# Kernel tuning notes

Measured on AMD Instinct MI355X. Metric: run time of the kernel, lower is better.

The kernel has to match this reference:

```python
import jax, jax.numpy as jnp
import numpy as np

B, T_ENC, H, L, OUT, S_DEC = 32, 512, 512, 2, 128, 128
KV = 2 * H  # bidirectional encoder output width


def setup_inputs() -> dict:
    key = jax.random.key(0)
    ks = jax.random.split(key, 17)
    s = 0.05  # keep recurrent dynamics stable
    return {
        "encoder_output": jax.random.normal(ks[0], (B, T_ENC, KV), jnp.float32),
        "h0": jax.random.normal(ks[1], (L, B, H), jnp.float32) * s,
        "c0": jax.random.normal(ks[2], (L, B, H), jnp.float32) * s,
        "Wk": jax.random.normal(ks[3], (KV, KV), jnp.float32) * s,
        "Wq": jax.random.normal(ks[4], (KV, H), jnp.float32) * s,
        "Wv": jax.random.normal(ks[5], (KV, KV), jnp.float32) * s,
        "We": jax.random.normal(ks[6], (1, KV), jnp.float32) * s,
        "wih0": jax.random.normal(ks[7], (4 * H, OUT + KV), jnp.float32) * s,
        "whh0": jax.random.normal(ks[8], (4 * H, H), jnp.float32) * s,
        "bih0": jax.random.normal(ks[9], (4 * H,), jnp.float32) * s,
        "bhh0": jax.random.normal(ks[10], (4 * H,), jnp.float32) * s,
        "wih1": jax.random.normal(ks[11], (4 * H, H), jnp.float32) * s,
        "whh1": jax.random.normal(ks[12], (4 * H, H), jnp.float32) * s,
        "bih1": jax.random.normal(ks[13], (4 * H,), jnp.float32) * s,
        "bhh1": jax.random.normal(ks[14], (4 * H,), jnp.float32) * s,
        "fc_w": jax.random.normal(ks[15], (OUT, H), jnp.float32) * s,
        "fc_b": jax.random.normal(ks[16], (OUT,), jnp.float32) * s,
        "seq_length": S_DEC,
    }


def _lstm_cell(x, h, c, wih, whh, bih, bhh):
    # torch gate order: i, f, g, o
    g = x @ wih.T + h @ whh.T + bih + bhh
    i, f, gg, o = jnp.split(g, 4, axis=-1)
    c_new = jax.nn.sigmoid(f) * c + jax.nn.sigmoid(i) * jnp.tanh(gg)
    h_new = jax.nn.sigmoid(o) * jnp.tanh(c_new)
    return h_new, c_new


def reference(encoder_output, h0, c0, Wk, Wq, Wv, We, wih0, whh0, bih0, bhh0,
              wih1, whh1, bih1, bhh1, fc_w, fc_b, seq_length):
    # precomputed projections (key_layer / value_layer, no bias)
    key = encoder_output @ Wk.T      # [B, T_enc, KV]
    value = encoder_output @ Wv.T    # [B, T_enc, KV]

    def step(carry, _):
        h, c, y = carry  # h,c: [L,B,H]; y: [B,OUT]
        # Bahdanau attention, query = layer-0 hidden state
        q = h[0] @ Wq.T                                         # [B, KV]
        scores = jnp.einsum('btk,k->bt', jnp.tanh(q[:, None, :] + key), We[0])
        alpha = jax.nn.softmax(scores, axis=-1)                 # [B, T_enc]
        context = jnp.einsum('bt,btd->bd', alpha, value)        # [B, KV]
        x = jnp.concatenate([y, context], axis=-1)              # [B, OUT+KV]
        h0n, c0n = _lstm_cell(x, h[0], c[0], wih0, whh0, bih0, bhh0)
        h1n, c1n = _lstm_cell(h0n, h[1], c[1], wih1, whh1, bih1, bhh1)
        y_hat = jax.nn.relu(h1n @ fc_w.T + fc_b)                # [B, OUT]
        new_carry = (jnp.stack([h0n, h1n]), jnp.stack([c0n, c1n]), 1.0 + y_hat)
        return new_carry, y_hat

    y_init = jnp.zeros((h0.shape[1], fc_b.shape[0]), jnp.float32)  # SOS = 0.0
    _, ys = jax.lax.scan(step, (h0, c0, y_init), None, length=seq_length)
    return jnp.transpose(ys, (1, 0, 2))  # [B, seq_length, OUT]
```

## Files before the change

### kernel.cpp

```cpp
#include <hip/hip_runtime.h>
#include <hip/hip_bf16.h>
#include <cstdint>

#define TE    512
#define SD    128

typedef unsigned short u16;
typedef u16 u16x4 __attribute__((ext_vector_type(4)));
typedef u16 u16x8 __attribute__((ext_vector_type(8)));

#define QO    0
#define SCO   32768
#define CTXO  81920
#define YO    114688
#define H0O   118784
#define C0O   151552
#define H1O   184320
#define C1O   217088
#define ST_N  249856

__device__ __forceinline__ float b2f(u16 v) { return __uint_as_float(((unsigned)v) << 16); }
__device__ __forceinline__ u16 f2b(float f) {
  unsigned u = __float_as_uint(f);
  return (u16)((u + 0x7FFFu + ((u >> 16) & 1u)) >> 16);
}
__device__ __forceinline__ float tanh_f(float x) {
  float xc = fminf(12.f, fmaxf(-12.f, x));
  float e  = __expf(2.f * xc);
  return __fdividef(e - 1.f, e + 1.f);
}
__device__ __forceinline__ float sigm(float x) {
  float xc = fminf(30.f, fmaxf(-30.f, x));
  return __fdividef(1.f, 1.f + __expf(-xc));
}

__global__ __launch_bounds__(256)
void gemm_kv(const float* __restrict__ E, const float* __restrict__ Wk,
             const float* __restrict__ Wv, u16* __restrict__ key, u16* __restrict__ value) {
  const float* B = blockIdx.z ? Wv : Wk;
  u16* outp = blockIdx.z ? value : key;
  __shared__ float Asm[16][68], Bsm[16][68];
  const int tid = threadIdx.x;
  const int tm = blockIdx.x * 64, tn = blockIdx.y * 64;
  const int lr = tid >> 2, lc = (tid & 3) * 4;
  const int tx = tid & 15, ty = tid >> 4;
  float acc[4][4] = {};
  for (int k0 = 0; k0 < 1024; k0 += 16) {
    float4 av = *(const float4*)(&E[(long)(tm + lr) * 1024 + k0 + lc]);
    float4 bv = *(const float4*)(&B[(long)(tn + lr) * 1024 + k0 + lc]);
    Asm[lc][lr] = av.x; Asm[lc + 1][lr] = av.y; Asm[lc + 2][lr] = av.z; Asm[lc + 3][lr] = av.w;
    Bsm[lc][lr] = bv.x; Bsm[lc + 1][lr] = bv.y; Bsm[lc + 2][lr] = bv.z; Bsm[lc + 3][lr] = bv.w;
    __syncthreads();
#pragma unroll
    for (int kk = 0; kk < 16; ++kk) {
      float4 a4 = *(const float4*)(&Asm[kk][ty * 4]);
      float4 b4 = *(const float4*)(&Bsm[kk][tx * 4]);
      acc[0][0] += a4.x * b4.x; acc[0][1] += a4.x * b4.y; acc[0][2] += a4.x * b4.z; acc[0][3] += a4.x * b4.w;
      acc[1][0] += a4.y * b4.x; acc[1][1] += a4.y * b4.y; acc[1][2] += a4.y * b4.z; acc[1][3] += a4.y * b4.w;
      acc[2][0] += a4.z * b4.x; acc[2][1] += a4.z * b4.y; acc[2][2] += a4.z * b4.z; acc[2][3] += a4.z * b4.w;
      acc[3][0] += a4.w * b4.x; acc[3][1] += a4.w * b4.y; acc[3][2] += a4.w * b4.z; acc[3][3] += a4.w * b4.w;
    }
    __syncthreads();
  }
#pragma unroll
  for (int i = 0; i < 4; ++i)
#pragma unroll
    for (int j = 0; j < 4; ++j)
      outp[(long)(tm + ty * 4 + i) * 1024 + tn + tx * 4 + j] = f2b(acc[i][j]);
}

__global__ __launch_bounds__(256)
void init_state(const float* __restrict__ h0, const float* __restrict__ c0, float* __restrict__ st) {
  int i = blockIdx.x * 256 + threadIdx.x;
  st[H0O + i] = h0[i];
  st[H1O + i] = h0[16384 + i];
  st[C0O + i] = c0[i];
  st[C1O + i] = c0[16384 + i];
  if (i < 4096) st[YO + i] = 0.f;
}

__global__ __launch_bounds__(256)
void qproj(const float* __restrict__ h0, const float* __restrict__ Wq, float* __restrict__ st) {
  __shared__ float hr[512];
  const int b = blockIdx.x >> 2, o = (blockIdx.x & 3) * 256 + threadIdx.x;
  for (int i = threadIdx.x; i < 512; i += 256) hr[i] = h0[b * 512 + i];
  __syncthreads();
  float acc = 0.f;
  for (int k = 0; k < 512; k += 4) {
    float4 wv = *(const float4*)(&Wq[(long)o * 512 + k]);
    acc += hr[k] * wv.x + hr[k + 1] * wv.y + hr[k + 2] * wv.z + hr[k + 3] * wv.w;
  }
  st[QO + b * 1024 + o] = acc;
}

__global__ __launch_bounds__(256)
void stepA(const u16* __restrict__ key, const float* __restrict__ We, float* __restrict__ st) {
  const int tid = threadIdx.x, wv = tid >> 6, ln = tid & 63;
  const int b = blockIdx.x >> 4, tc = blockIdx.x & 15, t0 = tc * 32;
  float qr[16], wer[16];
  {
    const float* qp = st + QO + b * 1024 + ln * 16;
#pragma unroll
    for (int j = 0; j < 16; ++j) qr[j] = qp[j];
#pragma unroll
    for (int j = 0; j < 16; j += 4) {
      float4 w4 = *(const float4*)(&We[ln * 16 + j]);
      wer[j] = w4.x; wer[j + 1] = w4.y; wer[j + 2] = w4.z; wer[j + 3] = w4.w;
    }
  }
  const u16* kbase = key + ((long)(b * TE + t0) << 10) + ln * 16;
#pragma unroll
  for (int u = 0; u < 4; ++u) {
    const int tt0 = wv + u * 8, tt1 = wv + u * 8 + 4;
    const u16* kr0 = kbase + ((long)tt0 << 10);
    const u16* kr1 = kbase + ((long)tt1 << 10);
    u16x8 a0 = *(const u16x8*)kr0, a1 = *(const u16x8*)(kr0 + 8);
    u16x8 b0 = *(const u16x8*)kr1, b1 = *(const u16x8*)(kr1 + 8);
    float p0 = 0.f, p1 = 0.f;
#pragma unroll
    for (int j = 0; j < 8; ++j) {
      p0 += tanh_f(qr[j] + b2f(a0[j])) * wer[j];
      p1 += tanh_f(qr[j] + b2f(b0[j])) * wer[j];
    }
#pragma unroll
    for (int j = 0; j < 8; ++j) {
      p0 += tanh_f(qr[8 + j] + b2f(a1[j])) * wer[8 + j];
      p1 += tanh_f(qr[8 + j] + b2f(b1[j])) * wer[8 + j];
    }
    for (int off = 32; off; off >>= 1) {
      p0 += __shfl_down(p0, off);
      p1 += __shfl_down(p1, off);
    }
    if (ln == 0) {
      st[SCO + b * 512 + t0 + tt0] = p0;
      st[SCO + b * 512 + t0 + tt1] = p1;
    }
  }
}

__global__ __launch_bounds__(256)
void stepB(const u16* __restrict__ value, const float* __restrict__ fcw,
           const float* __restrict__ fcb, float* __restrict__ st,
           float* __restrict__ out, int s) {
  __shared__ float sm[1576];
  const int tid = threadIdx.x, wv = tid >> 6, ln = tid & 63;
  if (blockIdx.x < 256) {
    const int b = blockIdx.x >> 3, dc = blockIdx.x & 7;
    float* al = sm; float* rr = sm + 512; float* gp = sm + 520;
    al[tid]       = st[SCO + b * 512 + tid];
    al[tid + 256] = st[SCO + b * 512 + tid + 256];
    __syncthreads();
    float m = fmaxf(al[tid], al[tid + 256]);
    for (int off = 32; off; off >>= 1) m = fmaxf(m, __shfl_xor(m, off));
    if (ln == 0) rr[wv] = m;
    __syncthreads();
    const float M = fmaxf(fmaxf(rr[0], rr[1]), fmaxf(rr[2], rr[3]));
    float e0 = __expf(al[tid] - M), e1 = __expf(al[tid + 256] - M);
    float l = e0 + e1;
    for (int off = 32; off; off >>= 1) l += __shfl_xor(l, off);
    if (ln == 0) rr[4 + wv] = l;
    __syncthreads();
    const float inv = __fdividef(1.f, rr[4] + rr[5] + rr[6] + rr[7]);
    al[tid] = e0; al[tid + 256] = e1;
    __syncthreads();
    const int dl = (tid & 31) * 4, tg = tid >> 5;
    float a0 = 0.f, a1 = 0.f, a2 = 0.f, a3 = 0.f;
    const u16* vb = value + ((long)(b * TE) << 10) + dc * 128 + dl;
#pragma unroll 4
    for (int t = tg; t < 512; t += 8) {
      u16x4 vvv = *(const u16x4*)(vb + ((long)t << 10));
      float av = al[t];
      a0 += av * b2f(vvv[0]); a1 += av * b2f(vvv[1]);
      a2 += av * b2f(vvv[2]); a3 += av * b2f(vvv[3]);
    }
    float4 a4 = {a0, a1, a2, a3};
    *(float4*)(&gp[tg * 132 + dl]) = a4;
    __syncthreads();
    if (tid < 128) {
      float ssum = 0.f;
#pragma unroll
      for (int g = 0; g < 8; ++g) ssum += gp[g * 132 + tid];
      st[CTXO + b * 1024 + dc * 128 + tid] = ssum * inv;
    }
  } else if (s > 0) {
    float* h1s = sm;
    const int b = blockIdx.x - 256;
    const int p = s & 1;
    for (int i = tid; i < 512; i += 256) h1s[i] = st[H1O + p * 16384 + b * 512 + i];
    __syncthreads();
#pragma unroll
    for (int oi = 0; oi < 32; ++oi) {
      const int o = wv * 32 + oi;
      float part = 0.f;
#pragma unroll
      for (int kk = 0; kk < 8; ++kk) {
        int k = kk * 64 + ln;
        part += h1s[k] * fcw[(long)o * 512 + k];
      }
      for (int off = 32; off; off >>= 1) part += __shfl_down(part, off);
      if (ln == 0) {
        float yh = fmaxf(part + fcb[o], 0.f);
        out[((long)b * SD + (s - 1)) * 128 + o] = yh;
        st[YO + b * 128 + o] = 1.f + yh;
      }
    }
  }
}

__global__ __launch_bounds__(256)
void stepC(const float* __restrict__ wih0, const float* __restrict__ whh0,
           const float* __restrict__ bih0, const float* __restrict__ bhh0,
           float* __restrict__ st, int p) {
  __shared__ float xs[32 * 132];
  __shared__ float wr[8 * 132];
  __shared__ float gp[4 * 32 * 8];
  const int tid = threadIdx.x, wv = tid >> 6, ln = tid & 63;
  const int h0d = blockIdx.x * 2;
  float acc[8];
#pragma unroll
  for (int r = 0; r < 8; ++r) acc[r] = 0.f;
  for (int ch = 0; ch < 13; ++ch) {
    const float* src; int stride, col0;
    if (ch == 0)      { src = st + YO;               stride = 128;  col0 = 0; }
    else if (ch <= 8) { src = st + CTXO;             stride = 1024; col0 = (ch - 1) * 128; }
    else              { src = st + H0O + p * 16384;  stride = 512;  col0 = (ch - 9) * 128; }
#pragma unroll
    for (int i = 0; i < 4; ++i) {
      int e4 = tid * 4 + i * 1024;
      int bs = e4 >> 7, j = e4 & 127;
      *(float4*)(&xs[bs * 132 + j]) = *(const float4*)(src + bs * stride + col0 + j);
    }
    {
      int e = tid * 4, r = e >> 7, j = e & 127;
      int g = r >> 1, hh = r & 1;
      const float* wsrc; long rb;
      if (ch <= 8) { wsrc = wih0; rb = (long)(g * 512 + h0d + hh) * 1152 + ch * 128; }
      else         { wsrc = whh0; rb = (long)(g * 512 + h0d + hh) * 512 + (ch - 9) * 128; }
      *(float4*)(&wr[r * 132 + j]) = *(const float4*)(&wsrc[rb + j]);
    }
    __syncthreads();
    const int b = tid & 31, j0 = (tid >> 5) * 16;
#pragma unroll
    for (int jj = 0; jj < 16; jj += 4) {
      const float4 xv = *(const float4*)(&xs[b * 132 + j0 + jj]);
#pragma unroll
      for (int r = 0; r < 8; ++r) {
        const float4 w4 = *(const float4*)(&wr[r * 132 + j0 + jj]);
        acc[r] += xv.x * w4.x + xv.y * w4.y + xv.z * w4.z + xv.w * w4.w;
      }
    }
    __syncthreads();
  }
#pragma unroll
  for (int r = 0; r < 8; ++r) acc[r] += __shfl_down(acc[r], 32);
  if (ln < 32) {
#pragma unroll
    for (int r = 0; r < 8; ++r) gp[(wv * 32 + ln) * 8 + r] = acc[r];
  }
  __syncthreads();
  if (tid < 64) {
    const int b = tid & 31, hh = tid >> 5, h = h0d + hh;
    float gg[4];
#pragma unroll
    for (int g = 0; g < 4; ++g) {
      int r = g * 2 + hh;
      gg[g] = gp[(0 * 32 + b) * 8 + r] + gp[(1 * 32 + b) * 8 + r] +
              gp[(2 * 32 + b) * 8 + r] + gp[(3 * 32 + b) * 8 + r] +
              bih0[g * 512 + h] + bhh0[g * 512 + h];
    }
    float ig = sigm(gg[0]), fg = sigm(gg[1]), gt = tanh_f(gg[2]), og = sigm(gg[3]);
    int si = b * 512 + h;
    float c  = st[C0O + p * 16384 + si];
    float cn = fg * c + ig * gt;
    float hn = og * tanh_f(cn);
    st[H0O + (p ^ 1) * 16384 + si] = hn;
    st[C0O + (p ^ 1) * 16384 + si] = cn;
  }
}

__global__ __launch_bounds__(256)
void stepD(const float* __restrict__ wih1, const float* __restrict__ whh1,
           const float* __restrict__ bih1, const float* __restrict__ bhh1,
           const float* __restrict__ Wq, float* __restrict__ st, int p) {
  __shared__ float xs[32 * 132];
  __shared__ float wr[12 * 132];
  __shared__ float gp[4 * 32 * 12];
  const int tid = threadIdx.x, wv = tid >> 6, ln = tid & 63;
  const int h0d = blockIdx.x * 2;
  float acc[12];
#pragma unroll
  for (int r = 0; r < 12; ++r) acc[r] = 0.f;
  for (int ch = 0; ch < 8; ++ch) {
    const float* src = (ch < 4) ? (st + H0O + (p ^ 1) * 16384) : (st + H1O + p * 16384);
    const int col0 = (ch & 3) * 128;
#pragma unroll
    for (int i = 0; i < 4; ++i) {
      int e4 = tid * 4 + i * 1024;
      int bs = e4 >> 7, j = e4 & 127;
      *(float4*)(&xs[bs * 132 + j]) = *(const float4*)(src + bs * 512 + col0 + j);
    }
    {
      int e = tid * 4, r = e >> 7, j = e & 127;
      int g = r >> 1, hh = r & 1;
      const float* wsrc = (ch < 4) ? wih1 : whh1;
      long rb = (long)(g * 512 + h0d + hh) * 512 + col0;
      *(float4*)(&wr[r * 132 + j]) = *(const float4*)(&wsrc[rb + j]);
      if (ch < 4 && tid < 128) {
        int rq = e >> 7, j2 = e & 127;
        long rqb = (long)(4 * blockIdx.x + rq) * 512 + col0;
        *(float4*)(&wr[(8 + rq) * 132 + j2]) = *(const float4*)(&Wq[rqb + j2]);
      }
    }
    __syncthreads();
    const int b = tid & 31, j0 = (tid >> 5) * 16;
#pragma unroll
    for (int jj = 0; jj < 16; jj += 4) {
      const float4 xv = *(const float4*)(&xs[b * 132 + j0 + jj]);
#pragma unroll
      for (int r = 0; r < 8; ++r) {
        const float4 w4 = *(const float4*)(&wr[r * 132 + j0 + jj]);
        acc[r] += xv.x * w4.x + xv.y * w4.y + xv.z * w4.z + xv.w * w4.w;
      }
      if (ch < 4) {
#pragma unroll
        for (int r = 8; r < 12; ++r) {
          const float4 w4 = *(const float4*)(&wr[r * 132 + j0 + jj]);
          acc[r] += xv.x * w4.x + xv.y * w4.y + xv.z * w4.z + xv.w * w4.w;
        }
      }
    }
    __syncthreads();
  }
#pragma unroll
  for (int r = 0; r < 12; ++r) acc[r] += __shfl_down(acc[r], 32);
  if (ln < 32) {
#pragma unroll
    for (int r = 0; r < 12; ++r) gp[(wv * 32 + ln) * 12 + r] = acc[r];
  }
  __syncthreads();
  if (tid < 64) {
    const int b = tid & 31, hh = tid >> 5, h = h0d + hh;
    float gg[4];
#pragma unroll
    for (int g = 0; g < 4; ++g) {
      int r = g * 2 + hh;
      gg[g] = gp[(0 * 32 + b) * 12 + r] + gp[(1 * 32 + b) * 12 + r] +
              gp[(2 * 32 + b) * 12 + r] + gp[(3 * 32 + b) * 12 + r] +
              bih1[g * 512 + h] + bhh1[g * 512 + h];
    }
    float ig = sigm(gg[0]), fg = sigm(gg[1]), gt = tanh_f(gg[2]), og = sigm(gg[3]);
    int si = b * 512 + h;
    float c  = st[C1O + p * 16384 + si];
    float cn = fg * c + ig * gt;
    float hn = og * tanh_f(cn);
    st[H1O + (p ^ 1) * 16384 + si] = hn;
    st[C1O + (p ^ 1) * 16384 + si] = cn;
    int r0 = 8 + 2 * hh;
    float q0 = gp[(0 * 32 + b) * 12 + r0]     + gp[(1 * 32 + b) * 12 + r0] +
               gp[(2 * 32 + b) * 12 + r0]     + gp[(3 * 32 + b) * 12 + r0];
    float q1 = gp[(0 * 32 + b) * 12 + r0 + 1] + gp[(1 * 32 + b) * 12 + r0 + 1] +
               gp[(2 * 32 + b) * 12 + r0 + 1] + gp[(3 * 32 + b) * 12 + r0 + 1];
    int o0 = 4 * blockIdx.x + 2 * hh;
    st[QO + b * 1024 + o0]     = q0;
    st[QO + b * 1024 + o0 + 1] = q1;
  }
}

__global__ __launch_bounds__(256)
void fcK(const float* __restrict__ fcw, const float* __restrict__ fcb,
         float* __restrict__ st, float* __restrict__ out) {
  __shared__ float h1s[512];
  const int b = blockIdx.x >> 2, og = (blockIdx.x & 3) * 32;
  const int tid = threadIdx.x, wv = tid >> 6, ln = tid & 63;
  for (int i = tid; i < 512; i += 256) h1s[i] = st[H1O + b * 512 + i];
  __syncthreads();
#pragma unroll
  for (int oi = 0; oi < 8; ++oi) {
    const int o = og + wv * 8 + oi;
    float part = 0.f;
#pragma unroll
    for (int kk = 0; kk < 8; ++kk) {
      int k = kk * 64 + ln;
      part += h1s[k] * fcw[(long)o * 512 + k];
    }
    for (int off = 32; off; off >>= 1) part += __shfl_down(part, off);
    if (ln == 0) {
      float yh = fmaxf(part + fcb[o], 0.f);
      out[((long)b * SD + (SD - 1)) * 128 + o] = yh;
    }
  }
}

extern "C" void kernel_launch(void* const* d_in, const int* in_sizes, int n_in,
                              void* d_out, int out_size, void* d_ws, size_t ws_size,
                              hipStream_t stream) {
  (void)in_sizes; (void)n_in; (void)out_size; (void)ws_size;
  float* out = (float*)d_out;

  const float* E    = (const float*)d_in[0];
  const float* h0   = (const float*)d_in[1];
  const float* c0   = (const float*)d_in[2];
  const float* Wk   = (const float*)d_in[3];
  const float* Wq   = (const float*)d_in[4];
  const float* Wv   = (const float*)d_in[5];
  const float* We   = (const float*)d_in[6];
  const float* wih0 = (const float*)d_in[7];
  const float* whh0 = (const float*)d_in[8];
  const float* bih0 = (const float*)d_in[9];
  const float* bhh0 = (const float*)d_in[10];
  const float* wih1 = (const float*)d_in[11];
  const float* whh1 = (const float*)d_in[12];
  const float* bih1 = (const float*)d_in[13];
  const float* bhh1 = (const float*)d_in[14];
  const float* fcw  = (const float*)d_in[15];
  const float* fcb  = (const float*)d_in[16];

  u16* key   = (u16*)d_ws;
  u16* value = key + 16777216;
  float* st  = (float*)d_ws + 16777216;

  gemm_kv<<<dim3(256, 16, 2), 256, 0, stream>>>(E, Wk, Wv, key, value);
  init_state<<<64, 256, 0, stream>>>(h0, c0, st);
  qproj<<<128, 256, 0, stream>>>(h0, Wq, st);

  for (int s = 0; s < SD; ++s) {
    int p = s & 1;
    stepA<<<512, 256, 0, stream>>>(key, We, st);
    stepB<<<288, 256, 0, stream>>>(value, fcw, fcb, st, out, s);
    stepC<<<256, 256, 0, stream>>>(wih0, whh0, bih0, bhh0, st, p);
    stepD<<<256, 256, 0, stream>>>(wih1, whh1, bih1, bhh1, Wq, st, p);
  }
  fcK<<<128, 256, 0, stream>>>(fcw, fcb, st, out);
}
```

Baseline: 12.01 ms.

## Fuse per-step decoder kernels into one persistent kernel with grid barriers

```diff
diff --git a/kernel.cpp b/kernel.cpp
--- a/kernel.cpp
+++ b/kernel.cpp
@@ -1,5 +1,4 @@
 #include <hip/hip_runtime.h>
-#include <hip/hip_bf16.h>
 #include <cstdint>
 
 #define TE    512
@@ -11,13 +10,13 @@
 
 #define QO    0
 #define SCO   32768
+#define BARO  49152
 #define CTXO  81920
 #define YO    114688
 #define H0O   118784
 #define C0O   151552
 #define H1O   184320
 #define C1O   217088
-#define ST_N  249856
 
 __device__ __forceinline__ float b2f(u16 v) { return __uint_as_float(((unsigned)v) << 16); }
 __device__ __forceinline__ u16 f2b(float f) {
@@ -77,6 +76,7 @@
   st[C0O + i] = c0[i];
   st[C1O + i] = c0[16384 + i];
   if (i < 4096) st[YO + i] = 0.f;
+  if (i == 0) *(unsigned*)(st + BARO) = 0u;
 }
 
 __global__ __launch_bounds__(256)
@@ -93,104 +93,310 @@
   st[QO + b * 1024 + o] = acc;
 }
 
-__global__ __launch_bounds__(256)
-void stepA(const u16* __restrict__ key, const float* __restrict__ We, float* __restrict__ st) {
+__global__ __launch_bounds__(256, 2)
+void decode_loop(const u16* __restrict__ key, const u16* __restrict__ value,
+                 const float* __restrict__ We,
+                 const float* __restrict__ wih0, const float* __restrict__ whh0,
+                 const float* __restrict__ bih0, const float* __restrict__ bhh0,
+                 const float* __restrict__ wih1, const float* __restrict__ whh1,
+                 const float* __restrict__ bih1, const float* __restrict__ bhh1,
+                 const float* __restrict__ Wq,
+                 const float* __restrict__ fcw, const float* __restrict__ fcb,
+                 float* st, float* out) {
+  __shared__ float smem[7344];
   const int tid = threadIdx.x, wv = tid >> 6, ln = tid & 63;
-  const int b = blockIdx.x >> 4, tc = blockIdx.x & 15, t0 = tc * 32;
-  float qr[16], wer[16];
-  {
-    const float* qp = st + QO + b * 1024 + ln * 16;
-#pragma unroll
-    for (int j = 0; j < 16; ++j) qr[j] = qp[j];
-#pragma unroll
-    for (int j = 0; j < 16; j += 4) {
-      float4 w4 = *(const float4*)(&We[ln * 16 + j]);
-      wer[j] = w4.x; wer[j + 1] = w4.y; wer[j + 2] = w4.z; wer[j + 3] = w4.w;
-    }
+  const int bid = blockIdx.x;
+  unsigned* bar = (unsigned*)(st + BARO);
+  unsigned bt = 0;
+
+#define GBAR() do {                                                                   \
+    ++bt;                                                                             \
+    __syncthreads();                                                                  \
+    if (tid == 0) {                                                                   \
+      __threadfence();                                                                \
+      __hip_atomic_fetch_add(bar, 1u, __ATOMIC_RELAXED, __HIP_MEMORY_SCOPE_AGENT);    \
+      while (__hip_atomic_load(bar, __ATOMIC_RELAXED, __HIP_MEMORY_SCOPE_AGENT)       \
+             < bt * 256u) { __builtin_amdgcn_s_sleep(1); }                            \
+      __threadfence();                                                                \
+    }                                                                                 \
+    __syncthreads();                                                                  \
+  } while (0)
+
+  float wer[16];
+#pragma unroll
+  for (int j = 0; j < 16; j += 4) {
+    float4 w4 = *(const float4*)(&We[ln * 16 + j]);
+    wer[j] = w4.x; wer[j + 1] = w4.y; wer[j + 2] = w4.z; wer[j + 3] = w4.w;
   }
-  const u16* kbase = key + ((long)(b * TE + t0) << 10) + ln * 16;
-#pragma unroll
-  for (int u = 0; u < 4; ++u) {
-    const int tt0 = wv + u * 8, tt1 = wv + u * 8 + 4;
-    const u16* kr0 = kbase + ((long)tt0 << 10);
-    const u16* kr1 = kbase + ((long)tt1 << 10);
-    u16x8 a0 = *(const u16x8*)kr0, a1 = *(const u16x8*)(kr0 + 8);
-    u16x8 b0 = *(const u16x8*)kr1, b1 = *(const u16x8*)(kr1 + 8);
-    float p0 = 0.f, p1 = 0.f;
-#pragma unroll
-    for (int j = 0; j < 8; ++j) {
-      p0 += tanh_f(qr[j] + b2f(a0[j])) * wer[j];
-      p1 += tanh_f(qr[j] + b2f(b0[j])) * wer[j];
-    }
-#pragma unroll
-    for (int j = 0; j < 8; ++j) {
-      p0 += tanh_f(qr[8 + j] + b2f(a1[j])) * wer[8 + j];
-      p1 += tanh_f(qr[8 + j] + b2f(b1[j])) * wer[8 + j];
-    }
-    for (int off = 32; off; off >>= 1) {
-      p0 += __shfl_down(p0, off);
-      p1 += __shfl_down(p1, off);
-    }
-    if (ln == 0) {
-      st[SCO + b * 512 + t0 + tt0] = p0;
-      st[SCO + b * 512 + t0 + tt1] = p1;
-    }
+
+  for (int s = 0; s < SD; ++s) {
+    const int p = s & 1;
+
+    for (int u = bid; u < 512; u += 256) {
+      const int ab = u >> 4, at0 = (u & 15) * 32;
+      const u16* kbase = key + ((long)(ab * TE + at0) << 10) + ln * 16;
+      float qr[16];
+      const float* qp = st + QO + ab * 1024 + ln * 16;
+#pragma unroll
+      for (int j = 0; j < 16; j += 4) {
+        float4 q4 = *(const float4*)(qp + j);
+        qr[j] = q4.x; qr[j + 1] = q4.y; qr[j + 2] = q4.z; qr[j + 3] = q4.w;
+      }
+#pragma unroll
+      for (int uu = 0; uu < 4; ++uu) {
+        const int tt0 = wv + uu * 8, tt1 = wv + uu * 8 + 4;
+        const u16* kr0 = kbase + ((long)tt0 << 10);
+        const u16* kr1 = kbase + ((long)tt1 << 10);
+        u16x8 a0 = *(const u16x8*)kr0, a1 = *(const u16x8*)(kr0 + 8);
+        u16x8 b0 = *(const u16x8*)kr1, b1 = *(const u16x8*)(kr1 + 8);
+        float p0 = 0.f, p1 = 0.f;
+#pragma unroll
+        for (int j = 0; j < 8; ++j) {
+          p0 += tanh_f(qr[j] + b2f(a0[j])) * wer[j];
+          p1 += tanh_f(qr[j] + b2f(b0[j])) * wer[j];
+        }
+#pragma unroll
+        for (int j = 0; j < 8; ++j) {
+          p0 += tanh_f(qr[8 + j] + b2f(a1[j])) * wer[8 + j];
+          p1 += tanh_f(qr[8 + j] + b2f(b1[j])) * wer[8 + j];
+        }
+        for (int off = 32; off; off >>= 1) {
+          p0 += __shfl_down(p0, off);
+          p1 += __shfl_down(p1, off);
+        }
+        if (ln == 0) {
+          st[SCO + ab * 512 + at0 + tt0] = p0;
+          st[SCO + ab * 512 + at0 + tt1] = p1;
+        }
+      }
+    }
+    if (bid < 32 && s > 0) {
+      float* h1s = smem;
+      const int b = bid;
+      for (int i = tid; i < 512; i += 256) h1s[i] = st[H1O + p * 16384 + b * 512 + i];
+      __syncthreads();
+#pragma unroll
+      for (int oi = 0; oi < 32; ++oi) {
+        const int o = wv * 32 + oi;
+        float part = 0.f;
+#pragma unroll
+        for (int kk = 0; kk < 8; ++kk) {
+          int k = kk * 64 + ln;
+          part += h1s[k] * fcw[(long)o * 512 + k];
+        }
+        for (int off = 32; off; off >>= 1) part += __shfl_down(part, off);
+        if (ln == 0) {
+          float yh = fmaxf(part + fcb[o], 0.f);
+          out[((long)b * SD + (s - 1)) * 128 + o] = yh;
+          st[YO + b * 128 + o] = 1.f + yh;
+        }
+      }
+    }
+    GBAR();
+
+    {
+      const int b = bid >> 3, dc = bid & 7;
+      float* al = smem; float* rr = smem + 512; float* gp = smem + 520;
+      al[tid]       = st[SCO + b * 512 + tid];
+      al[tid + 256] = st[SCO + b * 512 + tid + 256];
+      __syncthreads();
+      float m = fmaxf(al[tid], al[tid + 256]);
+      for (int off = 32; off; off >>= 1) m = fmaxf(m, __shfl_xor(m, off));
+      if (ln == 0) rr[wv] = m;
+      __syncthreads();
+      const float M = fmaxf(fmaxf(rr[0], rr[1]), fmaxf(rr[2], rr[3]));
+      float e0 = __expf(al[tid] - M), e1 = __expf(al[tid + 256] - M);
+      float l = e0 + e1;
+      for (int off = 32; off; off >>= 1) l += __shfl_xor(l, off);
+      if (ln == 0) rr[4 + wv] = l;
+      __syncthreads();
+      const float inv = __fdividef(1.f, rr[4] + rr[5] + rr[6] + rr[7]);
+      al[tid] = e0; al[tid + 256] = e1;
+      __syncthreads();
+      const int dl = (tid & 31) * 4, tg = tid >> 5;
+      float a0 = 0.f, a1 = 0.f, a2 = 0.f, a3 = 0.f;
+      const u16* vb = value + ((long)(b * TE) << 10) + dc * 128 + dl;
+#pragma unroll 4
+      for (int t = tg; t < 512; t += 8) {
+        u16x4 vvv = *(const u16x4*)(vb + ((long)t << 10));
+        float av = al[t];
+        a0 += av * b2f(vvv[0]); a1 += av * b2f(vvv[1]);
+        a2 += av * b2f(vvv[2]); a3 += av * b2f(vvv[3]);
+      }
+      float4 a4 = {a0, a1, a2, a3};
+      *(float4*)(&gp[tg * 132 + dl]) = a4;
+      __syncthreads();
+      if (tid < 128) {
+        float ssum = 0.f;
+#pragma unroll
+        for (int g = 0; g < 8; ++g) ssum += gp[g * 132 + tid];
+        st[CTXO + b * 1024 + dc * 128 + tid] = ssum * inv;
+      }
+    }
+    GBAR();
+
+    {
+      float* xs = smem;
+      float* wr = smem + 4224;
+      float* gp = smem + 5280;
+      const int h0d = bid * 2;
+      float acc[8];
+#pragma unroll
+      for (int r = 0; r < 8; ++r) acc[r] = 0.f;
+      for (int ch = 0; ch < 13; ++ch) {
+        const float* src; int stride, col0;
+        if (ch == 0)      { src = st + YO;               stride = 128;  col0 = 0; }
+        else if (ch <= 8) { src = st + CTXO;             stride = 1024; col0 = (ch - 1) * 128; }
+        else              { src = st + H0O + p * 16384;  stride = 512;  col0 = (ch - 9) * 128; }
+#pragma unroll
+        for (int i = 0; i < 4; ++i) {
+          int e4 = tid * 4 + i * 1024;
+          int bs = e4 >> 7, j = e4 & 127;
+          *(float4*)(&xs[bs * 132 + j]) = *(const float4*)(src + bs * stride + col0 + j);
+        }
+        {
+          int e = tid * 4, r = e >> 7, j = e & 127;
+          int g = r >> 1, hh = r & 1;
+          const float* wsrc; long rb;
+          if (ch <= 8) { wsrc = wih0; rb = (long)(g * 512 + h0d + hh) * 1152 + ch * 128; }
+          else         { wsrc = whh0; rb = (long)(g * 512 + h0d + hh) * 512 + (ch - 9) * 128; }
+          *(float4*)(&wr[r * 132 + j]) = *(const float4*)(&wsrc[rb + j]);
+        }
+        __syncthreads();
+        const int b = tid & 31, j0 = (tid >> 5) * 16;
+#pragma unroll
+        for (int jj = 0; jj < 16; jj += 4) {
+          const float4 xv = *(const float4*)(&xs[b * 132 + j0 + jj]);
+#pragma unroll
+          for (int r = 0; r < 8; ++r) {
+            const float4 w4 = *(const float4*)(&wr[r * 132 + j0 + jj]);
+            acc[r] += xv.x * w4.x + xv.y * w4.y + xv.z * w4.z + xv.w * w4.w;
+          }
+        }
+        __syncthreads();
+      }
+#pragma unroll
+      for (int r = 0; r < 8; ++r) acc[r] += __shfl_down(acc[r], 32);
+      if (ln < 32) {
+#pragma unroll
+        for (int r = 0; r < 8; ++r) gp[(wv * 32 + ln) * 8 + r] = acc[r];
+      }
+      __syncthreads();
+      if (tid < 64) {
+        const int b = tid & 31, hh = tid >> 5, h = h0d + hh;
+        float gg[4];
+#pragma unroll
+        for (int g = 0; g < 4; ++g) {
+          int r = g * 2 + hh;
+          gg[g] = gp[(0 * 32 + b) * 8 + r] + gp[(1 * 32 + b) * 8 + r] +
+                  gp[(2 * 32 + b) * 8 + r] + gp[(3 * 32 + b) * 8 + r] +
+                  bih0[g * 512 + h] + bhh0[g * 512 + h];
+        }
+        float ig = sigm(gg[0]), fg = sigm(gg[1]), gt = tanh_f(gg[2]), og = sigm(gg[3]);
+        int si = b * 512 + h;
+        float c  = st[C0O + p * 16384 + si];
+        float cn = fg * c + ig * gt;
+        float hn = og * tanh_f(cn);
+        st[H0O + (p ^ 1) * 16384 + si] = hn;
+        st[C0O + (p ^ 1) * 16384 + si] = cn;
+      }
+    }
+    GBAR();
+
+    {
+      float* xs = smem;
+      float* wr = smem + 4224;
+      float* gp = smem + 5808;
+      const int h0d = bid * 2;
+      float acc[12];
+#pragma unroll
+      for (int r = 0; r < 12; ++r) acc[r] = 0.f;
+      for (int ch = 0; ch < 8; ++ch) {
+        const float* src = (ch < 4) ? (st + H0O + (p ^ 1) * 16384) : (st + H1O + p * 16384);
+        const int col0 = (ch & 3) * 128;
+#pragma unroll
+        for (int i = 0; i < 4; ++i) {
+          int e4 = tid * 4 + i * 1024;
+          int bs = e4 >> 7, j = e4 & 127;
+          *(float4*)(&xs[bs * 132 + j]) = *(const float4*)(src + bs * 512 + col0 + j);
+        }
+        {
+          int e = tid * 4, r = e >> 7, j = e & 127;
+          int g = r >> 1, hh = r & 1;
+          const float* wsrc = (ch < 4) ? wih1 : whh1;
+          long rb = (long)(g * 512 + h0d + hh) * 512 + col0;
+          *(float4*)(&wr[r * 132 + j]) = *(const float4*)(&wsrc[rb + j]);
+          if (ch < 4 && tid < 128) {
+            int rq = e >> 7, j2 = e & 127;
+            long rqb = (long)(4 * bid + rq) * 512 + col0;
+            *(float4*)(&wr[(8 + rq) * 132 + j2]) = *(const float4*)(&Wq[rqb + j2]);
+          }
+        }
+        __syncthreads();
+        const int b = tid & 31, j0 = (tid >> 5) * 16;
+#pragma unroll
+        for (int jj = 0; jj < 16; jj += 4) {
+          const float4 xv = *(const float4*)(&xs[b * 132 + j0 + jj]);
+#pragma unroll
+          for (int r = 0; r < 8; ++r) {
+            const float4 w4 = *(const float4*)(&wr[r * 132 + j0 + jj]);
+            acc[r] += xv.x * w4.x + xv.y * w4.y + xv.z * w4.z + xv.w * w4.w;
+          }
+          if (ch < 4) {
+#pragma unroll
+            for (int r = 8; r < 12; ++r) {
+              const float4 w4 = *(const float4*)(&wr[r * 132 + j0 + jj]);
+              acc[r] += xv.x * w4.x + xv.y * w4.y + xv.z * w4.z + xv.w * w4.w;
+            }
+          }
+        }
+        __syncthreads();
+      }
+#pragma unroll
+      for (int r = 0; r < 12; ++r) acc[r] += __shfl_down(acc[r], 32);
+      if (ln < 32) {
+#pragma unroll
+        for (int r = 0; r < 12; ++r) gp[(wv * 32 + ln) * 12 + r] = acc[r];
+      }
+      __syncthreads();
+      if (tid < 64) {
+        const int b = tid & 31, hh = tid >> 5, h = h0d + hh;
+        float gg[4];
+#pragma unroll
+        for (int g = 0; g < 4; ++g) {
+          int r = g * 2 + hh;
+          gg[g] = gp[(0 * 32 + b) * 12 + r] + gp[(1 * 32 + b) * 12 + r] +
+                  gp[(2 * 32 + b) * 12 + r] + gp[(3 * 32 + b) * 12 + r] +
+                  bih1[g * 512 + h] + bhh1[g * 512 + h];
+        }
+        float ig = sigm(gg[0]), fg = sigm(gg[1]), gt = tanh_f(gg[2]), og = sigm(gg[3]);
+        int si = b * 512 + h;
+        float c  = st[C1O + p * 16384 + si];
+        float cn = fg * c + ig * gt;
+        float hn = og * tanh_f(cn);
+        st[H1O + (p ^ 1) * 16384 + si] = hn;
+        st[C1O + (p ^ 1) * 16384 + si] = cn;
+        int r0 = 8 + 2 * hh;
+        float q0 = gp[(0 * 32 + b) * 12 + r0]     + gp[(1 * 32 + b) * 12 + r0] +
+                   gp[(2 * 32 + b) * 12 + r0]     + gp[(3 * 32 + b) * 12 + r0];
+        float q1 = gp[(0 * 32 + b) * 12 + r0 + 1] + gp[(1 * 32 + b) * 12 + r0 + 1] +
+                   gp[(2 * 32 + b) * 12 + r0 + 1] + gp[(3 * 32 + b) * 12 + r0 + 1];
+        int o0 = 4 * bid + 2 * hh;
+        st[QO + b * 1024 + o0]     = q0;
+        st[QO + b * 1024 + o0 + 1] = q1;
+      }
+    }
+    GBAR();
   }
-}
-
-__global__ __launch_bounds__(256)
-void stepB(const u16* __restrict__ value, const float* __restrict__ fcw,
-           const float* __restrict__ fcb, float* __restrict__ st,
-           float* __restrict__ out, int s) {
-  __shared__ float sm[1576];
-  const int tid = threadIdx.x, wv = tid >> 6, ln = tid & 63;
-  if (blockIdx.x < 256) {
-    const int b = blockIdx.x >> 3, dc = blockIdx.x & 7;
-    float* al = sm; float* rr = sm + 512; float* gp = sm + 520;
-    al[tid]       = st[SCO + b * 512 + tid];
-    al[tid + 256] = st[SCO + b * 512 + tid + 256];
+
+  if (bid < 128) {
+    float* h1s = smem;
+    const int b = bid >> 2, og = (bid & 3) * 32;
+    for (int i = tid; i < 512; i += 256) h1s[i] = st[H1O + b * 512 + i];
     __syncthreads();
-    float m = fmaxf(al[tid], al[tid + 256]);
-    for (int off = 32; off; off >>= 1) m = fmaxf(m, __shfl_xor(m, off));
-    if (ln == 0) rr[wv] = m;
-    __syncthreads();
-    const float M = fmaxf(fmaxf(rr[0], rr[1]), fmaxf(rr[2], rr[3]));
-    float e0 = __expf(al[tid] - M), e1 = __expf(al[tid + 256] - M);
-    float l = e0 + e1;
-    for (int off = 32; off; off >>= 1) l += __shfl_xor(l, off);
-    if (ln == 0) rr[4 + wv] = l;
-    __syncthreads();
-    const float inv = __fdividef(1.f, rr[4] + rr[5] + rr[6] + rr[7]);
-    al[tid] = e0; al[tid + 256] = e1;
-    __syncthreads();
-    const int dl = (tid & 31) * 4, tg = tid >> 5;
-    float a0 = 0.f, a1 = 0.f, a2 = 0.f, a3 = 0.f;
-    const u16* vb = value + ((long)(b * TE) << 10) + dc * 128 + dl;
-#pragma unroll 4
-    for (int t = tg; t < 512; t += 8) {
-      u16x4 vvv = *(const u16x4*)(vb + ((long)t << 10));
-      float av = al[t];
-      a0 += av * b2f(vvv[0]); a1 += av * b2f(vvv[1]);
-      a2 += av * b2f(vvv[2]); a3 += av * b2f(vvv[3]);
-    }
-    float4 a4 = {a0, a1, a2, a3};
-    *(float4*)(&gp[tg * 132 + dl]) = a4;
-    __syncthreads();
-    if (tid < 128) {
-      float ssum = 0.f;
-#pragma unroll
-      for (int g = 0; g < 8; ++g) ssum += gp[g * 132 + tid];
-      st[CTXO + b * 1024 + dc * 128 + tid] = ssum * inv;
-    }
-  } else if (s > 0) {
-    float* h1s = sm;
-    const int b = blockIdx.x - 256;
-    const int p = s & 1;
-    for (int i = tid; i < 512; i += 256) h1s[i] = st[H1O + p * 16384 + b * 512 + i];
-    __syncthreads();
-#pragma unroll
-    for (int oi = 0; oi < 32; ++oi) {
-      const int o = wv * 32 + oi;
+#pragma unroll
+    for (int oi = 0; oi < 8; ++oi) {
+      const int o = og + wv * 8 + oi;
       float part = 0.f;
 #pragma unroll
       for (int kk = 0; kk < 8; ++kk) {
@@ -200,195 +406,11 @@
       for (int off = 32; off; off >>= 1) part += __shfl_down(part, off);
       if (ln == 0) {
         float yh = fmaxf(part + fcb[o], 0.f);
-        out[((long)b * SD + (s - 1)) * 128 + o] = yh;
-        st[YO + b * 128 + o] = 1.f + yh;
+        out[((long)b * SD + (SD - 1)) * 128 + o] = yh;
       }
     }
   }
-}
-
-__global__ __launch_bounds__(256)
-void stepC(const float* __restrict__ wih0, const float* __restrict__ whh0,
-           const float* __restrict__ bih0, const float* __restrict__ bhh0,
-           float* __restrict__ st, int p) {
-  __shared__ float xs[32 * 132];
-  __shared__ float wr[8 * 132];
-  __shared__ float gp[4 * 32 * 8];
-  const int tid = threadIdx.x, wv = tid >> 6, ln = tid & 63;
-  const int h0d = blockIdx.x * 2;
-  float acc[8];
-#pragma unroll
-  for (int r = 0; r < 8; ++r) acc[r] = 0.f;
-  for (int ch = 0; ch < 13; ++ch) {
-    const float* src; int stride, col0;
-    if (ch == 0)      { src = st + YO;               stride = 128;  col0 = 0; }
-    else if (ch <= 8) { src = st + CTXO;             stride = 1024; col0 = (ch - 1) * 128; }
-    else              { src = st + H0O + p * 16384;  stride = 512;  col0 = (ch - 9) * 128; }
-#pragma unroll
-    for (int i = 0; i < 4; ++i) {
-      int e4 = tid * 4 + i * 1024;
-      int bs = e4 >> 7, j = e4 & 127;
-      *(float4*)(&xs[bs * 132 + j]) = *(const float4*)(src + bs * stride + col0 + j);
-    }
-    {
-      int e = tid * 4, r = e >> 7, j = e & 127;
-      int g = r >> 1, hh = r & 1;
-      const float* wsrc; long rb;
-      if (ch <= 8) { wsrc = wih0; rb = (long)(g * 512 + h0d + hh) * 1152 + ch * 128; }
-      else         { wsrc = whh0; rb = (long)(g * 512 + h0d + hh) * 512 + (ch - 9) * 128; }
-      *(float4*)(&wr[r * 132 + j]) = *(const float4*)(&wsrc[rb + j]);
-    }
-    __syncthreads();
-    const int b = tid & 31, j0 = (tid >> 5) * 16;
-#pragma unroll
-    for (int jj = 0; jj < 16; jj += 4) {
-      const float4 xv = *(const float4*)(&xs[b * 132 + j0 + jj]);
-#pragma unroll
-      for (int r = 0; r < 8; ++r) {
-        const float4 w4 = *(const float4*)(&wr[r * 132 + j0 + jj]);
-        acc[r] += xv.x * w4.x + xv.y * w4.y + xv.z * w4.z + xv.w * w4.w;
-      }
-    }
-    __syncthreads();
-  }
-#pragma unroll
-  for (int r = 0; r < 8; ++r) acc[r] += __shfl_down(acc[r], 32);
-  if (ln < 32) {
-#pragma unroll
-    for (int r = 0; r < 8; ++r) gp[(wv * 32 + ln) * 8 + r] = acc[r];
-  }
-  __syncthreads();
-  if (tid < 64) {
-    const int b = tid & 31, hh = tid >> 5, h = h0d + hh;
-    float gg[4];
-#pragma unroll
-    for (int g = 0; g < 4; ++g) {
-      int r = g * 2 + hh;
-      gg[g] = gp[(0 * 32 + b) * 8 + r] + gp[(1 * 32 + b) * 8 + r] +
-              gp[(2 * 32 + b) * 8 + r] + gp[(3 * 32 + b) * 8 + r] +
-              bih0[g * 512 + h] + bhh0[g * 512 + h];
-    }
-    float ig = sigm(gg[0]), fg = sigm(gg[1]), gt = tanh_f(gg[2]), og = sigm(gg[3]);
-    int si = b * 512 + h;
-    float c  = st[C0O + p * 16384 + si];
-    float cn = fg * c + ig * gt;
-    float hn = og * tanh_f(cn);
-    st[H0O + (p ^ 1) * 16384 + si] = hn;
-    st[C0O + (p ^ 1) * 16384 + si] = cn;
-  }
-}
-
-__global__ __launch_bounds__(256)
-void stepD(const float* __restrict__ wih1, const float* __restrict__ whh1,
-           const float* __restrict__ bih1, const float* __restrict__ bhh1,
-           const float* __restrict__ Wq, float* __restrict__ st, int p) {
-  __shared__ float xs[32 * 132];
-  __shared__ float wr[12 * 132];
-  __shared__ float gp[4 * 32 * 12];
-  const int tid = threadIdx.x, wv = tid >> 6, ln = tid & 63;
-  const int h0d = blockIdx.x * 2;
-  float acc[12];
-#pragma unroll
-  for (int r = 0; r < 12; ++r) acc[r] = 0.f;
-  for (int ch = 0; ch < 8; ++ch) {
-    const float* src = (ch < 4) ? (st + H0O + (p ^ 1) * 16384) : (st + H1O + p * 16384);
-    const int col0 = (ch & 3) * 128;
-#pragma unroll
-    for (int i = 0; i < 4; ++i) {
-      int e4 = tid * 4 + i * 1024;
-      int bs = e4 >> 7, j = e4 & 127;
-      *(float4*)(&xs[bs * 132 + j]) = *(const float4*)(src + bs * 512 + col0 + j);
-    }
-    {
-      int e = tid * 4, r = e >> 7, j = e & 127;
-      int g = r >> 1, hh = r & 1;
-      const float* wsrc = (ch < 4) ? wih1 : whh1;
-      long rb = (long)(g * 512 + h0d + hh) * 512 + col0;
-      *(float4*)(&wr[r * 132 + j]) = *(const float4*)(&wsrc[rb + j]);
-      if (ch < 4 && tid < 128) {
-        int rq = e >> 7, j2 = e & 127;
-        long rqb = (long)(4 * blockIdx.x + rq) * 512 + col0;
-        *(float4*)(&wr[(8 + rq) * 132 + j2]) = *(const float4*)(&Wq[rqb + j2]);
-      }
-    }
-    __syncthreads();
-    const int b = tid & 31, j0 = (tid >> 5) * 16;
-#pragma unroll
-    for (int jj = 0; jj < 16; jj += 4) {
-      const float4 xv = *(const float4*)(&xs[b * 132 + j0 + jj]);
-#pragma unroll
-      for (int r = 0; r < 8; ++r) {
-        const float4 w4 = *(const float4*)(&wr[r * 132 + j0 + jj]);
-        acc[r] += xv.x * w4.x + xv.y * w4.y + xv.z * w4.z + xv.w * w4.w;
-      }
-      if (ch < 4) {
-#pragma unroll
-        for (int r = 8; r < 12; ++r) {
-          const float4 w4 = *(const float4*)(&wr[r * 132 + j0 + jj]);
-          acc[r] += xv.x * w4.x + xv.y * w4.y + xv.z * w4.z + xv.w * w4.w;
-        }
-      }
-    }
-    __syncthreads();
-  }
-#pragma unroll
-  for (int r = 0; r < 12; ++r) acc[r] += __shfl_down(acc[r], 32);
-  if (ln < 32) {
-#pragma unroll
-    for (int r = 0; r < 12; ++r) gp[(wv * 32 + ln) * 12 + r] = acc[r];
-  }
-  __syncthreads();
-  if (tid < 64) {
-    const int b = tid & 31, hh = tid >> 5, h = h0d + hh;
-    float gg[4];
-#pragma unroll
-    for (int g = 0; g < 4; ++g) {
-      int r = g * 2 + hh;
-      gg[g] = gp[(0 * 32 + b) * 12 + r] + gp[(1 * 32 + b) * 12 + r] +
-              gp[(2 * 32 + b) * 12 + r] + gp[(3 * 32 + b) * 12 + r] +
-              bih1[g * 512 + h] + bhh1[g * 512 + h];
-    }
-    float ig = sigm(gg[0]), fg = sigm(gg[1]), gt = tanh_f(gg[2]), og = sigm(gg[3]);
-    int si = b * 512 + h;
-    float c  = st[C1O + p * 16384 + si];
-    float cn = fg * c + ig * gt;
-    float hn = og * tanh_f(cn);
-    st[H1O + (p ^ 1) * 16384 + si] = hn;
-    st[C1O + (p ^ 1) * 16384 + si] = cn;
-    int r0 = 8 + 2 * hh;
-    float q0 = gp[(0 * 32 + b) * 12 + r0]     + gp[(1 * 32 + b) * 12 + r0] +
-               gp[(2 * 32 + b) * 12 + r0]     + gp[(3 * 32 + b) * 12 + r0];
-    float q1 = gp[(0 * 32 + b) * 12 + r0 + 1] + gp[(1 * 32 + b) * 12 + r0 + 1] +
-               gp[(2 * 32 + b) * 12 + r0 + 1] + gp[(3 * 32 + b) * 12 + r0 + 1];
-    int o0 = 4 * blockIdx.x + 2 * hh;
-    st[QO + b * 1024 + o0]     = q0;
-    st[QO + b * 1024 + o0 + 1] = q1;
-  }
-}
-
-__global__ __launch_bounds__(256)
-void fcK(const float* __restrict__ fcw, const float* __restrict__ fcb,
-         float* __restrict__ st, float* __restrict__ out) {
-  __shared__ float h1s[512];
-  const int b = blockIdx.x >> 2, og = (blockIdx.x & 3) * 32;
-  const int tid = threadIdx.x, wv = tid >> 6, ln = tid & 63;
-  for (int i = tid; i < 512; i += 256) h1s[i] = st[H1O + b * 512 + i];
-  __syncthreads();
-#pragma unroll
-  for (int oi = 0; oi < 8; ++oi) {
-    const int o = og + wv * 8 + oi;
-    float part = 0.f;
-#pragma unroll
-    for (int kk = 0; kk < 8; ++kk) {
-      int k = kk * 64 + ln;
-      part += h1s[k] * fcw[(long)o * 512 + k];
-    }
-    for (int off = 32; off; off >>= 1) part += __shfl_down(part, off);
-    if (ln == 0) {
-      float yh = fmaxf(part + fcb[o], 0.f);
-      out[((long)b * SD + (SD - 1)) * 128 + o] = yh;
-    }
-  }
+#undef GBAR
 }
 
 extern "C" void kernel_launch(void* const* d_in, const int* in_sizes, int n_in,
@@ -423,12 +445,8 @@
   init_state<<<64, 256, 0, stream>>>(h0, c0, st);
   qproj<<<128, 256, 0, stream>>>(h0, Wq, st);
 
-  for (int s = 0; s < SD; ++s) {
-    int p = s & 1;
-    stepA<<<512, 256, 0, stream>>>(key, We, st);
-    stepB<<<288, 256, 0, stream>>>(value, fcw, fcb, st, out, s);
-    stepC<<<256, 256, 0, stream>>>(wih0, whh0, bih0, bhh0, st, p);
-    stepD<<<256, 256, 0, stream>>>(wih1, whh1, bih1, bhh1, Wq, st, p);
-  }
-  fcK<<<128, 256, 0, stream>>>(fcw, fcb, st, out);
-}
+  decode_loop<<<256, 256, 0, stream>>>(key, value, We,
+                                       wih0, whh0, bih0, bhh0,
+                                       wih1, whh1, bih1, bhh1,
+                                       Wq, fcw, fcb, st, out);
+}
```

New measurement: 31.92 ms. +165.8%, slower.
